# Kernel tuning notes

Measured on AMD Instinct MI355X. Metric: run time of the kernel, lower is better.

The kernel has to match this reference:

```python
import jax, jax.numpy as jnp
import numpy as np

N_NODES = 50000
N_EDGES = 800000
IN_DIM = 128
HID_DIM = 128
NUM_GRAPHS = 64


def gcn_conv(x, edge_index, W, b):
    """PyG GCNConv: symmetric-normalized aggregation with self-loops.
    out = D^{-1/2} (A + I) D^{-1/2} (x @ W) + b
    """
    n = x.shape[0]
    loop = jnp.arange(n, dtype=edge_index.dtype)
    src = jnp.concatenate([edge_index[0], loop])  # [E+N]
    dst = jnp.concatenate([edge_index[1], loop])
    deg = jax.ops.segment_sum(jnp.ones_like(dst, x.dtype), dst, num_segments=n)
    dinv = jnp.where(deg > 0, jax.lax.rsqrt(deg), 0.0)
    norm = dinv[src] * dinv[dst]  # [E+N]
    h = x @ W  # [N, H] transform before propagate (PyG order)
    msg = h[src] * norm[:, None]  # [E+N, H] gathered+scaled messages
    out = jax.ops.segment_sum(msg, dst, num_segments=n)  # scatter-add
    return out + b


def global_mean_pool(x, batch, num_graphs):
    s = jax.ops.segment_sum(x, batch, num_segments=num_graphs)
    cnt = jax.ops.segment_sum(jnp.ones((x.shape[0],), x.dtype), batch, num_segments=num_graphs)
    return s / jnp.maximum(cnt, 1.0)[:, None]


def setup_inputs() -> dict:
    key = jax.random.key(0)
    ks = jax.random.split(key, 8)
    x = jax.random.normal(ks[0], (N_NODES, IN_DIM), dtype=jnp.float32)
    edge_index = jax.random.randint(ks[1], (2, N_EDGES), 0, N_NODES, dtype=jnp.int64)
    batch = jnp.sort(jax.random.randint(ks[2], (N_NODES,), 0, NUM_GRAPHS, dtype=jnp.int64))
    s1 = 1.0 / np.sqrt(IN_DIM)
    s2 = 1.0 / np.sqrt(HID_DIM)
    W1 = jax.random.uniform(ks[3], (IN_DIM, HID_DIM), jnp.float32, -s1, s1)
    b1 = jnp.zeros((HID_DIM,), jnp.float32)
    W2 = jax.random.uniform(ks[4], (HID_DIM, HID_DIM), jnp.float32, -s2, s2)
    b2 = jnp.zeros((HID_DIM,), jnp.float32)
    Wc = jax.random.uniform(ks[5], (HID_DIM, 1), jnp.float32, -s2, s2)
    bc = jnp.zeros((1,), jnp.float32)
    return {"x": x, "edge_index": edge_index, "batch": batch,
            "W1": W1, "b1": b1, "W2": W2, "b2": b2, "Wc": Wc, "bc": bc}


def reference(x, edge_index, batch, W1, b1, W2, b2, Wc, bc):
    h = jax.nn.relu(gcn_conv(x, edge_index, W1, b1))
    # dropout p=0.1 is identity in eval mode
    h = gcn_conv(h, edge_index, W2, b2)
    g = global_mean_pool(h, batch, NUM_GRAPHS)  # [G, H]
    return jax.nn.sigmoid(g @ Wc + bc)  # [G, 1]
```

## Files before the change

kernel.cpp:

```cpp
#include <hip/hip_runtime.h>
#include <hip/hip_bf16.h>
#include <hip/hip_fp16.h>

#define N_NODES 50000
#define N_EDGES 800000
#define DIM     128
#define NG      64
#define GN      16
#define CAP     48
#define AGG_EB  256
#define LAXP    136

#define NBIN    196
#define SORT_B  250
#define EPB     3200

#define CAST_B  1563
#define VB_B    129
#define WF_B    8

typedef float  f2_t  __attribute__((ext_vector_type(2)));
typedef float  f32x4 __attribute__((ext_vector_type(4)));
typedef _Float16 f16x8 __attribute__((ext_vector_type(8)));
typedef _Float16 f16x4 __attribute__((ext_vector_type(4)));

__global__ void k_prep(const int* __restrict__ ei, int* __restrict__ binCnt,
                       const float* __restrict__ W2, const float* __restrict__ Wc,
                       const float* __restrict__ b2, float* __restrict__ v,
                       float* __restrict__ beta2,
                       const float* __restrict__ W1, f16x8* __restrict__ w1f) {
    __shared__ float red[4];
    __shared__ int hist[256];
    int bid = blockIdx.x, t = threadIdx.x;
    if (bid < SORT_B) {
        hist[t] = 0;
        __syncthreads();
        int base = bid * EPB;
        for (int r = 0; r < 13; r++) {
            int idx = r * 256 + t;
            if (idx < EPB) {
                int d = ei[N_EDGES + base + idx];
                atomicAdd(&hist[d >> 8], 1);
            }
        }
        __syncthreads();
        if (t < NBIN && hist[t] > 0) atomicAdd(&binCnt[t], hist[t]);
    } else if (bid < SORT_B + VB_B) {
        int b = bid - SORT_B;
        float p = 0.f;
        if (t < DIM) p = (b < DIM) ? W2[b * DIM + t] * Wc[t] : b2[t] * Wc[t];
        #pragma unroll
        for (int off = 32; off > 0; off >>= 1) p += __shfl_down(p, off, 64);
        if ((t & 63) == 0) red[t >> 6] = p;
        __syncthreads();
        if (t == 0) {
            float s = red[0] + red[1];
            if (b < DIM) v[b] = s; else beta2[0] = s;
        }
    } else {
        int idx = (bid - (SORT_B + VB_B)) * 256 + t;
        int ntile = idx >> 8, kb = (idx >> 6) & 3, l = idx & 63;
        int kbase = kb * 32 + (l >> 4) * 8;
        int n = ntile * 16 + (l & 15);
        f16x8 o;
        #pragma unroll
        for (int j = 0; j < 8; j++) o[j] = (_Float16)W1[(kbase + j) * DIM + n];
        w1f[idx] = o;
    }
}

__global__ void k_scatter(const int* __restrict__ ei, const int* __restrict__ binCnt,
                          int* __restrict__ binCur, int* __restrict__ binOff,
                          unsigned int* __restrict__ sorted) {
    __shared__ int soff[256];
    __shared__ int hist[256];
    __shared__ int cur[256];
    int bid = blockIdx.x, t = threadIdx.x;
    int c = (t < NBIN) ? binCnt[t] : 0;
    soff[t] = c;
    #pragma unroll
    for (int o = 1; o < 256; o <<= 1) {
        __syncthreads();
        int v2 = (t >= o) ? soff[t - o] : 0;
        __syncthreads();
        soff[t] += v2;
    }
    __syncthreads();
    int excl = soff[t] - c;
    if (bid == 0 && t < NBIN) binOff[t] = excl;
    hist[t] = 0;
    __syncthreads();
    int base = bid * EPB;
    for (int r = 0; r < 13; r++) {
        int idx = r * 256 + t;
        if (idx < EPB) {
            int d = ei[N_EDGES + base + idx];
            atomicAdd(&hist[d >> 8], 1);
        }
    }
    __syncthreads();
    if (t < NBIN && hist[t] > 0) cur[t] = excl + atomicAdd(&binCur[t], hist[t]);
    __syncthreads();
    for (int r = 0; r < 13; r++) {
        int idx = r * 256 + t;
        if (idx < EPB) {
            int e = base + idx;
            int s = ei[e];
            int d = ei[N_EDGES + e];
            int pos = atomicAdd(&cur[d >> 8], 1);
            sorted[pos] = (unsigned)s | ((unsigned)(d & 255) << 16);
        }
    }
}

__global__ __launch_bounds__(512) void k_csr(const unsigned int* __restrict__ sorted,
                      const int* __restrict__ binOff, int* __restrict__ deg,
                      unsigned short* __restrict__ csr) {
    __shared__ int cur[256];
    int b = blockIdx.x, t = threadIdx.x;
    if (t < 256) cur[t] = 0;
    __syncthreads();
    int lo = binOff[b];
    int hi = (b == NBIN - 1) ? N_EDGES : binOff[b + 1];
    for (int i = lo + t; i < hi; i += 512) {
        unsigned e = sorted[i];
        unsigned src = e & 0xFFFFu;
        unsigned dLow = e >> 16;
        int pos = atomicAdd(&cur[dLow], 1);
        if (pos < CAP) csr[(size_t)(b * 256 + dLow) * CAP + pos] = (unsigned short)src;
    }
    __syncthreads();
    int node = b * 256 + t;
    if (t < 256 && node < N_NODES) deg[node] = cur[t];
}

__global__ void k_cast(const float4* __restrict__ x4, uint4* __restrict__ xq4,
                       const int* __restrict__ deg, const int* __restrict__ batch,
                       unsigned int* __restrict__ bd) {
    int idx = blockIdx.x * 256 + threadIdx.x;
    if (idx >= (N_NODES + 1) * 8) return;
    if (idx >= N_NODES * 8) {
        xq4[idx] = make_uint4(0u, 0u, 0u, 0u);
        return;
    }
    int node = idx >> 3;
    float di = rsqrtf((float)deg[node] + 1.f);
    uint4 o;
    unsigned* op = (unsigned*)&o;
    #pragma unroll
    for (int q = 0; q < 4; q++) {
        float4 f = x4[idx * 4 + q];
        int p = 0;
        p = __builtin_amdgcn_cvt_pk_fp8_f32(di * f.x, di * f.y, p, false);
        p = __builtin_amdgcn_cvt_pk_fp8_f32(di * f.z, di * f.w, p, true);
        op[q] = (unsigned)p;
    }
    xq4[idx] = o;
    if ((idx & 7) == 0) {
        unsigned hw = (unsigned)__half_as_ushort(__float2half(di));
        bd[node] = ((unsigned)batch[node] & 0xFFFFu) | (hw << 16);
    }
}

__global__ __launch_bounds__(512) void k_node(
    const unsigned int* __restrict__ xq,
    const unsigned short* __restrict__ csr,
    const f16x8* __restrict__ w1f,
    const float* __restrict__ b1,
    const float* __restrict__ v, const int* __restrict__ deg,
    float* __restrict__ z2) {
    __shared__ _Float16 laxh[GN * LAXP];
    __shared__ float redm[GN * 8];
    int tid = threadIdx.x;
    int w = tid >> 6, l = tid & 63;
    int half = l >> 5, hl = l & 31;
    int node0 = blockIdx.x * GN;

    {
        int i = node0 + 2 * w + half;
        int dg = deg[i];
        int len = min(dg, CAP);
        float di = rsqrtf((float)dg + 1.f);

        unsigned su = xq[(size_t)i * 32 + hl];
        f2_t s01 = __builtin_amdgcn_cvt_pk_f32_fp8((int)su, false);
        f2_t s23 = __builtin_amdgcn_cvt_pk_f32_fp8((int)su, true);
        float ax[8], ay[8], az[8], aw[8];
        #pragma unroll
        for (int k = 0; k < 8; k++) { ax[k] = 0.f; ay[k] = 0.f; az[k] = 0.f; aw[k] = 0.f; }
        ax[0] = s01.x; ay[0] = s01.y;
        az[0] = s23.x; aw[0] = s23.y;

        int lenmax = max(len, __shfl_xor(len, 32, 64));
        int lmp = (lenmax + 7) & ~7;
        const uint4* csr4 = (const uint4*)(csr + (size_t)i * CAP);
        for (int j = 0; j < lmp; j += 8) {
            uint4 cw = csr4[j >> 3];
            unsigned cw8[4] = {cw.x, cw.y, cw.z, cw.w};
            unsigned q[8];
            #pragma unroll
            for (int k = 0; k < 8; k++) {
                unsigned id = (cw8[k >> 1] >> ((k & 1) * 16)) & 0xFFFFu;
                unsigned idc = (j + k < len) ? id : (unsigned)N_NODES;
                q[k] = xq[(size_t)idc * 32 + hl];
            }
            #pragma unroll
            for (int k = 0; k < 8; k++) {
                f2_t e01 = __builtin_amdgcn_cvt_pk_f32_fp8((int)q[k], false);
                f2_t e23 = __builtin_amdgcn_cvt_pk_f32_fp8((int)q[k], true);
                ax[k] += e01.x; ay[k] += e01.y;
                az[k] += e23.x; aw[k] += e23.y;
            }
        }
        float a0 = 0.f, a1 = 0.f, a2 = 0.f, a3 = 0.f;
        #pragma unroll
        for (int k = 0; k < 8; k++) { a0 += ax[k]; a1 += ay[k]; a2 += az[k]; a3 += aw[k]; }
        f16x4 pk;
        pk[0] = (_Float16)(di * a0); pk[1] = (_Float16)(di * a1);
        pk[2] = (_Float16)(di * a2); pk[3] = (_Float16)(di * a3);
        *(f16x4*)&laxh[(2 * w + half) * LAXP + 4 * hl] = pk;
    }
    __syncthreads();

    f32x4 acc = {0.f, 0.f, 0.f, 0.f};
    #pragma unroll
    for (int kb = 0; kb < 4; kb++) {
        f16x8 af = *(const f16x8*)&laxh[(l & 15) * LAXP + kb * 32 + (l >> 4) * 8];
        f16x8 bf = w1f[(w * 4 + kb) * 64 + l];
        acc = __builtin_amdgcn_mfma_f32_16x16x32_f16(af, bf, acc, 0, 0, 0);
    }
    int n = w * 16 + (l & 15);
    float bn = b1[n], vn = v[n];
    #pragma unroll
    for (int r = 0; r < 4; r++) {
        float p = fmaxf(acc[r] + bn, 0.f) * vn;
        p += __shfl_xor(p, 1, 64);
        p += __shfl_xor(p, 2, 64);
        p += __shfl_xor(p, 4, 64);
        p += __shfl_xor(p, 8, 64);
        if ((l & 15) == 0) redm[((l >> 4) * 4 + r) * 8 + w] = p;
    }
    __syncthreads();
    if (tid < GN) {
        float s = 0.f;
        #pragma unroll
        for (int q = 0; q < 8; q++) s += redm[tid * 8 + q];
        z2[node0 + tid] = rsqrtf((float)deg[node0 + tid] + 1.f) * s;
    }
}

__global__ void k_aggz(const float* __restrict__ z2, const unsigned int* __restrict__ bd,
                       const int* __restrict__ ei, const int* __restrict__ batch,
                       float* __restrict__ gpartE, float* __restrict__ gpartN,
                       int* __restrict__ gcnt) {
    int bid = blockIdx.x, t = threadIdx.x;
    if (bid < AGG_EB) {
        __shared__ float bs[4][NG];
        bs[t >> 6][t & 63] = 0.f;
        __syncthreads();
        int wg = t >> 6;
        for (int base = bid * 1024; base < N_EDGES; base += AGG_EB * 1024) {
            #pragma unroll
            for (int k = 0; k < 4; k++) {
                int e = base + k * 256 + t;
                if (e < N_EDGES) {
                    int s = ei[e];
                    int d = ei[N_EDGES + e];
                    unsigned u = bd[d];
                    float dv = __half2float(__ushort_as_half((unsigned short)(u >> 16)));
                    atomicAdd(&bs[wg][u & 63u], dv * z2[s]);
                }
            }
        }
        __syncthreads();
        if (t < NG) gpartE[bid * NG + t] = bs[0][t] + bs[1][t] + bs[2][t] + bs[3][t];
    } else {
        __shared__ int range[2];
        __shared__ float rs[4];
        int g = bid - AGG_EB;
        if (t < 2) {
            int key = g + t;
            int lo = 0, hi = N_NODES;
            while (lo < hi) { int m = (lo + hi) >> 1; if (batch[m] < key) lo = m + 1; else hi = m; }
            range[t] = lo;
        }
        __syncthreads();
        int lo = range[0], hi = range[1];
        float loc = 0.f;
        for (int i = lo + t; i < hi; i += 256)
            loc += __half2float(__ushort_as_half((unsigned short)(bd[i] >> 16))) * z2[i];
        #pragma unroll
        for (int off = 32; off > 0; off >>= 1) loc += __shfl_down(loc, off, 64);
        if ((t & 63) == 0) rs[t >> 6] = loc;
        __syncthreads();
        if (t == 0) {
            gpartN[g] = rs[0] + rs[1] + rs[2] + rs[3];
            gcnt[g] = hi - lo;
        }
    }
}

__global__ void k_final(const float* __restrict__ gpartE, const float* __restrict__ gpartN,
                        const int* __restrict__ gcnt, const float* __restrict__ beta2,
                        const float* __restrict__ bcin, float* __restrict__ out) {
    __shared__ float acc[4][NG];
    int t = threadIdx.x;
    int g = t & 63, c = t >> 6;
    float s = 0.f;
    for (int k = 0; k < AGG_EB / 4; k++)
        s += gpartE[(c * (AGG_EB / 4) + k) * NG + g];
    acc[c][g] = s;
    __syncthreads();
    if (t < NG) {
        float tot = acc[0][t] + acc[1][t] + acc[2][t] + acc[3][t] + gpartN[t];
        int cnt = gcnt[t];
        float val = tot / (float)(cnt > 0 ? cnt : 1) + beta2[0] + bcin[0];
        out[t] = 1.f / (1.f + expf(-val));
    }
}

extern "C" void kernel_launch(void* const* d_in, const int* in_sizes, int n_in,
                              void* d_out, int out_size, void* d_ws, size_t ws_size,
                              hipStream_t stream) {
    const float* x   = (const float*)d_in[0];
    const int*   ei  = (const int*)  d_in[1];
    const int*   bat = (const int*)  d_in[2];
    const float* W1  = (const float*)d_in[3];
    const float* b1  = (const float*)d_in[4];
    const float* W2  = (const float*)d_in[5];
    const float* b2  = (const float*)d_in[6];
    const float* Wc  = (const float*)d_in[7];
    const float* bc  = (const float*)d_in[8];
    float* out = (float*)d_out;

    char* w = (char*)d_ws;
    size_t off = 0;
    auto alloc = [&](size_t bytes) -> void* {
        void* p = w + off;
        off = (off + bytes + 255) & ~(size_t)255;
        return p;
    };
    int*   binCnt  = (int*)  alloc(NBIN * 4);
    int*   binCur  = (int*)  alloc(NBIN * 4);
    size_t zero_len = off;
    int*   binOff  = (int*)  alloc(NBIN * 4);
    int*   deg     = (int*)  alloc(N_NODES * 4);
    float* z2      = (float*)alloc(N_NODES * 4);
    float* v       = (float*)alloc(DIM * 4);
    float* beta2   = (float*)alloc(4);
    float* gpartE  = (float*)alloc((size_t)AGG_EB * NG * 4);
    float* gpartN  = (float*)alloc(NG * 4);
    int*   gcnt    = (int*)  alloc(NG * 4);
    unsigned int* bd = (unsigned int*)alloc(N_NODES * 4);
    f16x8* w1f     = (f16x8*)alloc(2048 * 16);
    unsigned int* xq = (unsigned int*)alloc((size_t)(N_NODES + 1) * DIM);
    unsigned int* sorted = (unsigned int*)alloc((size_t)N_EDGES * 4);
    unsigned short* csr = (unsigned short*)alloc((size_t)N_NODES * CAP * 2);
    (void)ws_size; (void)in_sizes; (void)n_in; (void)out_size;

    hipMemsetAsync(d_ws, 0, zero_len, stream);

    dim3 b256(256);
    k_prep<<<dim3(SORT_B + VB_B + WF_B), b256, 0, stream>>>(
        ei, binCnt, W2, Wc, b2, v, beta2, W1, w1f);
    k_scatter<<<dim3(SORT_B), b256, 0, stream>>>(ei, binCnt, binCur, binOff, sorted);
    k_csr<<<dim3(NBIN), dim3(512), 0, stream>>>(sorted, binOff, deg, csr);
    k_cast<<<dim3(CAST_B), b256, 0, stream>>>(
        (const float4*)x, (uint4*)xq, deg, bat, bd);
    k_node<<<dim3(N_NODES / GN), dim3(512), 0, stream>>>(
        xq, csr, w1f, b1, v, deg, z2);
    k_aggz<<<dim3(AGG_EB + NG), b256, 0, stream>>>(z2, bd, ei, bat, gpartE, gpartN, gcnt);
    k_final<<<dim3(1), b256, 0, stream>>>(gpartE, gpartN, gcnt, beta2, bc, out);
}
```

Baseline: 165.9 us.

## Fuse cast into CSR build, reuse block histograms, fold final into aggregation

k_prep now saves each block's bin histogram so k_scatter no longer re-reads destinations and rebuilds it. The fp8 cast of x is merged into k_csr, which uses the shared-memory degree counts directly instead of rereading deg. k_final is removed: aggregation blocks atomically add into per-graph sums, and the last block, chosen by a ticket counter, computes the sigmoid output. This cuts two launches and one pass over the edge list, but k_csr now runs only 196 blocks for the cast work and float atomics make the summation order nondeterministic.

```diff
diff --git a/kernel.cpp b/kernel.cpp
--- a/kernel.cpp
+++ b/kernel.cpp
@@ -15,7 +15,6 @@
 #define SORT_B  250
 #define EPB     3200
 
-#define CAST_B  1563
 #define VB_B    129
 #define WF_B    8
 
@@ -25,6 +24,7 @@
 typedef _Float16 f16x4 __attribute__((ext_vector_type(4)));
 
 __global__ void k_prep(const int* __restrict__ ei, int* __restrict__ binCnt,
+                       int* __restrict__ blockHist,
                        const float* __restrict__ W2, const float* __restrict__ Wc,
                        const float* __restrict__ b2, float* __restrict__ v,
                        float* __restrict__ beta2,
@@ -44,7 +44,10 @@
             }
         }
         __syncthreads();
-        if (t < NBIN && hist[t] > 0) atomicAdd(&binCnt[t], hist[t]);
+        if (t < NBIN) {
+            blockHist[bid * 256 + t] = hist[t];
+            if (hist[t] > 0) atomicAdd(&binCnt[t], hist[t]);
+        }
     } else if (bid < SORT_B + VB_B) {
         int b = bid - SORT_B;
         float p = 0.f;
@@ -70,10 +73,10 @@
 }
 
 __global__ void k_scatter(const int* __restrict__ ei, const int* __restrict__ binCnt,
+                          const int* __restrict__ blockHist,
                           int* __restrict__ binCur, int* __restrict__ binOff,
                           unsigned int* __restrict__ sorted) {
     __shared__ int soff[256];
-    __shared__ int hist[256];
     __shared__ int cur[256];
     int bid = blockIdx.x, t = threadIdx.x;
     int c = (t < NBIN) ? binCnt[t] : 0;
@@ -88,19 +91,10 @@
     __syncthreads();
     int excl = soff[t] - c;
     if (bid == 0 && t < NBIN) binOff[t] = excl;
-    hist[t] = 0;
+    int myh = (t < NBIN) ? blockHist[bid * 256 + t] : 0;
+    if (myh > 0) cur[t] = excl + atomicAdd(&binCur[t], myh);
     __syncthreads();
     int base = bid * EPB;
-    for (int r = 0; r < 13; r++) {
-        int idx = r * 256 + t;
-        if (idx < EPB) {
-            int d = ei[N_EDGES + base + idx];
-            atomicAdd(&hist[d >> 8], 1);
-        }
-    }
-    __syncthreads();
-    if (t < NBIN && hist[t] > 0) cur[t] = excl + atomicAdd(&binCur[t], hist[t]);
-    __syncthreads();
     for (int r = 0; r < 13; r++) {
         int idx = r * 256 + t;
         if (idx < EPB) {
@@ -115,7 +109,9 @@
 
 __global__ __launch_bounds__(512) void k_csr(const unsigned int* __restrict__ sorted,
                       const int* __restrict__ binOff, int* __restrict__ deg,
-                      unsigned short* __restrict__ csr) {
+                      unsigned short* __restrict__ csr,
+                      const float4* __restrict__ x4, uint4* __restrict__ xq4,
+                      const int* __restrict__ batch, unsigned int* __restrict__ bd) {
     __shared__ int cur[256];
     int b = blockIdx.x, t = threadIdx.x;
     if (t < 256) cur[t] = 0;
@@ -130,36 +126,35 @@
         if (pos < CAP) csr[(size_t)(b * 256 + dLow) * CAP + pos] = (unsigned short)src;
     }
     __syncthreads();
-    int node = b * 256 + t;
-    if (t < 256 && node < N_NODES) deg[node] = cur[t];
-}
-
-__global__ void k_cast(const float4* __restrict__ x4, uint4* __restrict__ xq4,
-                       const int* __restrict__ deg, const int* __restrict__ batch,
-                       unsigned int* __restrict__ bd) {
-    int idx = blockIdx.x * 256 + threadIdx.x;
-    if (idx >= (N_NODES + 1) * 8) return;
-    if (idx >= N_NODES * 8) {
-        xq4[idx] = make_uint4(0u, 0u, 0u, 0u);
-        return;
-    }
-    int node = idx >> 3;
-    float di = rsqrtf((float)deg[node] + 1.f);
-    uint4 o;
-    unsigned* op = (unsigned*)&o;
+    if (t < 256) {
+        int node = b * 256 + t;
+        if (node < N_NODES) deg[node] = cur[t];
+    }
     #pragma unroll
-    for (int q = 0; q < 4; q++) {
-        float4 f = x4[idx * 4 + q];
-        int p = 0;
-        p = __builtin_amdgcn_cvt_pk_fp8_f32(di * f.x, di * f.y, p, false);
-        p = __builtin_amdgcn_cvt_pk_fp8_f32(di * f.z, di * f.w, p, true);
-        op[q] = (unsigned)p;
-    }
-    xq4[idx] = o;
-    if ((idx & 7) == 0) {
-        unsigned hw = (unsigned)__half_as_ushort(__float2half(di));
-        bd[node] = ((unsigned)batch[node] & 0xFFFFu) | (hw << 16);
-    }
+    for (int it = 0; it < 4; it++) {
+        int lin = it * 512 + t;
+        int nl = lin >> 3, j = lin & 7;
+        int node = b * 256 + nl;
+        if (node < N_NODES) {
+            float di = rsqrtf((float)cur[nl] + 1.f);
+            uint4 o;
+            unsigned* op = (unsigned*)&o;
+            #pragma unroll
+            for (int q = 0; q < 4; q++) {
+                float4 f = x4[(size_t)(node * 8 + j) * 4 + q];
+                int p = 0;
+                p = __builtin_amdgcn_cvt_pk_fp8_f32(di * f.x, di * f.y, p, false);
+                p = __builtin_amdgcn_cvt_pk_fp8_f32(di * f.z, di * f.w, p, true);
+                op[q] = (unsigned)p;
+            }
+            xq4[node * 8 + j] = o;
+            if (j == 0) {
+                unsigned hw = (unsigned)__half_as_ushort(__float2half(di));
+                bd[node] = ((unsigned)batch[node] & 0xFFFFu) | (hw << 16);
+            }
+        }
+    }
+    if (b == 0 && t < 8) xq4[N_NODES * 8 + t] = make_uint4(0u, 0u, 0u, 0u);
 }
 
 __global__ __launch_bounds__(512) void k_node(
@@ -251,8 +246,11 @@
 
 __global__ void k_aggz(const float* __restrict__ z2, const unsigned int* __restrict__ bd,
                        const int* __restrict__ ei, const int* __restrict__ batch,
-                       float* __restrict__ gpartE, float* __restrict__ gpartN,
-                       int* __restrict__ gcnt) {
+                       float* __restrict__ gsum, int* __restrict__ gcnt,
+                       int* __restrict__ ticket,
+                       const float* __restrict__ beta2, const float* __restrict__ bcin,
+                       float* __restrict__ out) {
+    __shared__ int isLast;
     int bid = blockIdx.x, t = threadIdx.x;
     if (bid < AGG_EB) {
         __shared__ float bs[4][NG];
@@ -273,7 +271,7 @@
             }
         }
         __syncthreads();
-        if (t < NG) gpartE[bid * NG + t] = bs[0][t] + bs[1][t] + bs[2][t] + bs[3][t];
+        if (t < NG) atomicAdd(&gsum[t], bs[0][t] + bs[1][t] + bs[2][t] + bs[3][t]);
     } else {
         __shared__ int range[2];
         __shared__ float rs[4];
@@ -294,27 +292,20 @@
         if ((t & 63) == 0) rs[t >> 6] = loc;
         __syncthreads();
         if (t == 0) {
-            gpartN[g] = rs[0] + rs[1] + rs[2] + rs[3];
-            gcnt[g] = hi - lo;
-        }
-    }
-}
-
-__global__ void k_final(const float* __restrict__ gpartE, const float* __restrict__ gpartN,
-                        const int* __restrict__ gcnt, const float* __restrict__ beta2,
-                        const float* __restrict__ bcin, float* __restrict__ out) {
-    __shared__ float acc[4][NG];
-    int t = threadIdx.x;
-    int g = t & 63, c = t >> 6;
-    float s = 0.f;
-    for (int k = 0; k < AGG_EB / 4; k++)
-        s += gpartE[(c * (AGG_EB / 4) + k) * NG + g];
-    acc[c][g] = s;
-    __syncthreads();
-    if (t < NG) {
-        float tot = acc[0][t] + acc[1][t] + acc[2][t] + acc[3][t] + gpartN[t];
-        int cnt = gcnt[t];
-        float val = tot / (float)(cnt > 0 ? cnt : 1) + beta2[0] + bcin[0];
+            atomicAdd(&gsum[g], rs[0] + rs[1] + rs[2] + rs[3]);
+            atomicAdd(&gcnt[g], hi - lo);
+        }
+    }
+    __threadfence();
+    if (t == 0) {
+        int old = atomicAdd(ticket, 1);
+        isLast = (old == AGG_EB + NG - 1) ? 1 : 0;
+    }
+    __syncthreads();
+    if (isLast && t < NG) {
+        float s = atomicAdd(&gsum[t], 0.f);
+        int cnt = atomicAdd(&gcnt[t], 0);
+        float val = s / (float)(cnt > 0 ? cnt : 1) + beta2[0] + bcin[0];
         out[t] = 1.f / (1.f + expf(-val));
     }
 }
@@ -342,17 +333,18 @@
     };
     int*   binCnt  = (int*)  alloc(NBIN * 4);
     int*   binCur  = (int*)  alloc(NBIN * 4);
+    float* gsum    = (float*)alloc(NG * 4);
+    int*   gcnt    = (int*)  alloc(NG * 4);
+    int*   ticket  = (int*)  alloc(4);
     size_t zero_len = off;
     int*   binOff  = (int*)  alloc(NBIN * 4);
     int*   deg     = (int*)  alloc(N_NODES * 4);
     float* z2      = (float*)alloc(N_NODES * 4);
     float* v       = (float*)alloc(DIM * 4);
     float* beta2   = (float*)alloc(4);
-    float* gpartE  = (float*)alloc((size_t)AGG_EB * NG * 4);
-    float* gpartN  = (float*)alloc(NG * 4);
-    int*   gcnt    = (int*)  alloc(NG * 4);
     unsigned int* bd = (unsigned int*)alloc(N_NODES * 4);
     f16x8* w1f     = (f16x8*)alloc(2048 * 16);
+    int*   blockHist = (int*)alloc((size_t)SORT_B * 256 * 4);
     unsigned int* xq = (unsigned int*)alloc((size_t)(N_NODES + 1) * DIM);
     unsigned int* sorted = (unsigned int*)alloc((size_t)N_EDGES * 4);
     unsigned short* csr = (unsigned short*)alloc((size_t)N_NODES * CAP * 2);
@@ -362,13 +354,13 @@
 
     dim3 b256(256);
     k_prep<<<dim3(SORT_B + VB_B + WF_B), b256, 0, stream>>>(
-        ei, binCnt, W2, Wc, b2, v, beta2, W1, w1f);
-    k_scatter<<<dim3(SORT_B), b256, 0, stream>>>(ei, binCnt, binCur, binOff, sorted);
-    k_csr<<<dim3(NBIN), dim3(512), 0, stream>>>(sorted, binOff, deg, csr);
-    k_cast<<<dim3(CAST_B), b256, 0, stream>>>(
-        (const float4*)x, (uint4*)xq, deg, bat, bd);
+        ei, binCnt, blockHist, W2, Wc, b2, v, beta2, W1, w1f);
+    k_scatter<<<dim3(SORT_B), b256, 0, stream>>>(
+        ei, binCnt, blockHist, binCur, binOff, sorted);
+    k_csr<<<dim3(NBIN), dim3(512), 0, stream>>>(
+        sorted, binOff, deg, csr, (const float4*)x, (uint4*)xq, bat, bd);
     k_node<<<dim3(N_NODES / GN), dim3(512), 0, stream>>>(
         xq, csr, w1f, b1, v, deg, z2);
-    k_aggz<<<dim3(AGG_EB + NG), b256, 0, stream>>>(z2, bd, ei, bat, gpartE, gpartN, gcnt);
-    k_final<<<dim3(1), b256, 0, stream>>>(gpartE, gpartN, gcnt, beta2, bc, out);
-}
+    k_aggz<<<dim3(AGG_EB + NG), b256, 0, stream>>>(
+        z2, bd, ei, bat, gsum, gcnt, ticket, beta2, bc, out);
+}
```

New measurement: 185.0 us. 11.5% more time.

## Aggregate layer-2 scalar via CSR gather instead of edge-list scatter

Applied to the files above, without the earlier changes.

The final scalar aggregation now reads z2 through the per-node CSR built earlier, gathering by destination node instead of streaming the raw edge list with shared-memory atomics. Each node's sum is binned by graph in shared memory, and blocks add their bins into a global 64-entry accumulator with atomics. The per-graph node-count binary search moves into the single-block final kernel. This drops reading the 6.4MB edge arrays and the separate node-pass blocks, at the cost of many global atomics and relying on CSR rows capped at CAP entries being complete.

```diff
diff --git a/kernel.cpp b/kernel.cpp
--- a/kernel.cpp
+++ b/kernel.cpp
@@ -8,7 +8,6 @@
 #define NG      64
 #define GN      16
 #define CAP     48
-#define AGG_EB  256
 #define LAXP    136
 
 #define NBIN    196
@@ -16,6 +15,7 @@
 #define EPB     3200
 
 #define CAST_B  1563
+#define ZAGG_B  1563
 #define VB_B    129
 #define WF_B    8
 
@@ -249,72 +249,50 @@
     }
 }
 
-__global__ void k_aggz(const float* __restrict__ z2, const unsigned int* __restrict__ bd,
-                       const int* __restrict__ ei, const int* __restrict__ batch,
-                       float* __restrict__ gpartE, float* __restrict__ gpartN,
-                       int* __restrict__ gcnt) {
-    int bid = blockIdx.x, t = threadIdx.x;
-    if (bid < AGG_EB) {
-        __shared__ float bs[4][NG];
-        bs[t >> 6][t & 63] = 0.f;
-        __syncthreads();
-        int wg = t >> 6;
-        for (int base = bid * 1024; base < N_EDGES; base += AGG_EB * 1024) {
-            #pragma unroll
-            for (int k = 0; k < 4; k++) {
-                int e = base + k * 256 + t;
-                if (e < N_EDGES) {
-                    int s = ei[e];
-                    int d = ei[N_EDGES + e];
-                    unsigned u = bd[d];
-                    float dv = __half2float(__ushort_as_half((unsigned short)(u >> 16)));
-                    atomicAdd(&bs[wg][u & 63u], dv * z2[s]);
-                }
-            }
-        }
-        __syncthreads();
-        if (t < NG) gpartE[bid * NG + t] = bs[0][t] + bs[1][t] + bs[2][t] + bs[3][t];
-    } else {
-        __shared__ int range[2];
-        __shared__ float rs[4];
-        int g = bid - AGG_EB;
-        if (t < 2) {
-            int key = g + t;
-            int lo = 0, hi = N_NODES;
-            while (lo < hi) { int m = (lo + hi) >> 1; if (batch[m] < key) lo = m + 1; else hi = m; }
-            range[t] = lo;
-        }
-        __syncthreads();
-        int lo = range[0], hi = range[1];
-        float loc = 0.f;
-        for (int i = lo + t; i < hi; i += 256)
-            loc += __half2float(__ushort_as_half((unsigned short)(bd[i] >> 16))) * z2[i];
-        #pragma unroll
-        for (int off = 32; off > 0; off >>= 1) loc += __shfl_down(loc, off, 64);
-        if ((t & 63) == 0) rs[t >> 6] = loc;
-        __syncthreads();
-        if (t == 0) {
-            gpartN[g] = rs[0] + rs[1] + rs[2] + rs[3];
-            gcnt[g] = hi - lo;
-        }
-    }
-}
-
-__global__ void k_final(const float* __restrict__ gpartE, const float* __restrict__ gpartN,
-                        const int* __restrict__ gcnt, const float* __restrict__ beta2,
-                        const float* __restrict__ bcin, float* __restrict__ out) {
-    __shared__ float acc[4][NG];
+__global__ __launch_bounds__(256) void k_zagg(
+    const float* __restrict__ z2, const unsigned int* __restrict__ bd,
+    const unsigned short* __restrict__ csr, const int* __restrict__ deg,
+    float* __restrict__ gsum) {
+    __shared__ float bins[4][NG];
+    int tid = threadIdx.x;
+    int w = tid >> 6, l = tid & 63;
+    int sg = l >> 3, sl = l & 7;
+    bins[w][l] = 0.f;
+    __syncthreads();
+    int node = blockIdx.x * 32 + w * 8 + sg;
+    if (node < N_NODES) {
+        int len = min(deg[node], CAP);
+        const unsigned short* row = csr + (size_t)node * CAP;
+        float s = 0.f;
+        for (int r = sl; r < len; r += 8)
+            s += z2[row[r]];
+        s += __shfl_xor(s, 1, 64);
+        s += __shfl_xor(s, 2, 64);
+        s += __shfl_xor(s, 4, 64);
+        if (sl == 0) {
+            unsigned u = bd[node];
+            float dv = __half2float(__ushort_as_half((unsigned short)(u >> 16)));
+            atomicAdd(&bins[w][u & 63u], dv * (s + z2[node]));
+        }
+    }
+    __syncthreads();
+    if (tid < NG) {
+        float s = bins[0][tid] + bins[1][tid] + bins[2][tid] + bins[3][tid];
+        if (s != 0.f) atomicAdd(&gsum[tid], s);
+    }
+}
+
+__global__ void k_final(const float* __restrict__ gsum, const int* __restrict__ batch,
+                        const float* __restrict__ beta2, const float* __restrict__ bcin,
+                        float* __restrict__ out) {
     int t = threadIdx.x;
-    int g = t & 63, c = t >> 6;
-    float s = 0.f;
-    for (int k = 0; k < AGG_EB / 4; k++)
-        s += gpartE[(c * (AGG_EB / 4) + k) * NG + g];
-    acc[c][g] = s;
-    __syncthreads();
     if (t < NG) {
-        float tot = acc[0][t] + acc[1][t] + acc[2][t] + acc[3][t] + gpartN[t];
-        int cnt = gcnt[t];
-        float val = tot / (float)(cnt > 0 ? cnt : 1) + beta2[0] + bcin[0];
+        int lo0 = 0, hi0 = N_NODES;
+        while (lo0 < hi0) { int m = (lo0 + hi0) >> 1; if (batch[m] < t) lo0 = m + 1; else hi0 = m; }
+        int lo1 = 0, hi1 = N_NODES;
+        while (lo1 < hi1) { int m = (lo1 + hi1) >> 1; if (batch[m] < t + 1) lo1 = m + 1; else hi1 = m; }
+        int cnt = lo1 - lo0;
+        float val = gsum[t] / (float)(cnt > 0 ? cnt : 1) + beta2[0] + bcin[0];
         out[t] = 1.f / (1.f + expf(-val));
     }
 }
@@ -342,15 +320,13 @@
     };
     int*   binCnt  = (int*)  alloc(NBIN * 4);
     int*   binCur  = (int*)  alloc(NBIN * 4);
+    float* gsum    = (float*)alloc(NG * 4);
     size_t zero_len = off;
     int*   binOff  = (int*)  alloc(NBIN * 4);
     int*   deg     = (int*)  alloc(N_NODES * 4);
     float* z2      = (float*)alloc(N_NODES * 4);
     float* v       = (float*)alloc(DIM * 4);
     float* beta2   = (float*)alloc(4);
-    float* gpartE  = (float*)alloc((size_t)AGG_EB * NG * 4);
-    float* gpartN  = (float*)alloc(NG * 4);
-    int*   gcnt    = (int*)  alloc(NG * 4);
     unsigned int* bd = (unsigned int*)alloc(N_NODES * 4);
     f16x8* w1f     = (f16x8*)alloc(2048 * 16);
     unsigned int* xq = (unsigned int*)alloc((size_t)(N_NODES + 1) * DIM);
@@ -369,6 +345,6 @@
         (const float4*)x, (uint4*)xq, deg, bat, bd);
     k_node<<<dim3(N_NODES / GN), dim3(512), 0, stream>>>(
         xq, csr, w1f, b1, v, deg, z2);
-    k_aggz<<<dim3(AGG_EB + NG), b256, 0, stream>>>(z2, bd, ei, bat, gpartE, gpartN, gcnt);
-    k_final<<<dim3(1), b256, 0, stream>>>(gpartE, gpartN, gcnt, beta2, bc, out);
-}
+    k_zagg<<<dim3(ZAGG_B), b256, 0, stream>>>(z2, bd, csr, deg, gsum);
+    k_final<<<dim3(1), dim3(64), 0, stream>>>(gsum, bat, beta2, bc, out);
+}
```

Measured after the change: 176.1 us. 6.1% more time.
